# Kernel optimization log

Measured on AMD Instinct MI355X. Metric: run time of the kernel, lower is better.

## Reference

```python
import jax, jax.numpy as jnp
import numpy as np

HW = 16          # feature map side before crop
P = HW * HW      # 256 spatial positions
G = 128          # output genetic channels per branch
CROP = 14        # crop size


def feature_genetic(x, idx, oh, ow):
    # x: [B, C, 16, 16]; idx: [G, P] channel index per (group, position);
    # oh, ow: [G] crop offsets in {0,1}
    B = x.shape[0]
    feat = x.reshape(B, x.shape[1], P)                 # [B, C, 256]
    pos = jnp.arange(P)
    picked = feat[:, idx, pos]                         # [B, G, 256]
    grid = picked.reshape(B, G, HW, HW)                # [B, 128, 16, 16]
    ch = jnp.arange(G)
    hidx = oh[:, None] + jnp.arange(CROP)[None, :]     # [G, 14]
    widx = ow[:, None] + jnp.arange(CROP)[None, :]     # [G, 14]
    # fancy-index crop: [B, 128, 14, 14]
    return grid[:, ch[:, None, None], hidx[:, :, None], widx[:, None, :]]


def setup_inputs() -> dict:
    key = jax.random.key(0)
    k1, k3, k5, kw, ki, kh, kw2 = jax.random.split(key, 7)
    B, C = 128, 512
    x1 = jax.random.normal(k1, (B, C, HW, HW), dtype=jnp.float32)
    x3 = jax.random.normal(k3, (B, C, HW, HW), dtype=jnp.float32)
    x5 = jax.random.normal(k5, (B, C, HW, HW), dtype=jnp.float32)
    W = jax.random.normal(kw, (768, 384), dtype=jnp.float32) * 0.02  # 1x1 conv weight
    idx = jax.random.randint(ki, (3, G, P), 0, C, dtype=jnp.int32)
    offh = jax.random.randint(kh, (3, G), 0, 2, dtype=jnp.int32)
    offw = jax.random.randint(kw2, (3, G), 0, 2, dtype=jnp.int32)
    return {"x1": x1, "x3": x3, "x5": x5, "W": W, "idx": idx, "offh": offh, "offw": offw}


def reference(x1, x3, x5, W, idx, offh, offw):
    g1 = feature_genetic(x1, idx[0], offh[0], offw[0])   # [B, 128, 14, 14]
    g3 = feature_genetic(x3, idx[1], offh[1], offw[1])
    g5 = feature_genetic(x5, idx[2], offh[2], offw[2])
    feats = jnp.concatenate((g1, g3, g5), axis=1)        # [B, 384, 14, 14]
    # 1x1 conv (no bias): Conv2d(384, 768, kernel_size=1)
    out = jnp.einsum('bchw,oc->bohw', feats, W)          # [B, 768, 14, 14]
    return out
```

## Files before the change

kernel.cpp:

```cpp
#include <hip/hip_runtime.h>
#include <hip/hip_bf16.h>

#define PIX 256
#define CROP 14
#define HW2 196
#define BB 128
#define CC 512
#define NC 384
#define NO 768
#define CAP 128
#define ENT_T 25088

typedef __bf16 bf16x8 __attribute__((ext_vector_type(8)));
typedef __bf16 bf16x4 __attribute__((ext_vector_type(4)));
typedef float  f32x4  __attribute__((ext_vector_type(4)));
typedef unsigned int u32;

#define GLOAD_LDS16(src, dst) \
    __builtin_amdgcn_global_load_lds((const __attribute__((address_space(1))) void*)(src), \
                                     (__attribute__((address_space(3))) void*)(dst), 16, 0, 0)

__global__ void wconv_kernel(const float* __restrict__ W, __bf16* __restrict__ Wb) {
    int tid = blockIdx.x * 256 + threadIdx.x;
    Wb[tid] = (__bf16)W[tid];
}

__global__ void fill_kernel(const int* __restrict__ idx, const int* __restrict__ offh,
                            const int* __restrict__ offw, int* __restrict__ cnt,
                            u32* __restrict__ bucket) {
    int tid = blockIdx.x * 256 + threadIdx.x;
    int c3 = tid / HW2;
    int hw = tid - c3 * HW2;
    int i = hw / CROP, j = hw - i * CROP;
    int p = (offh[c3] + i) * 16 + offw[c3] + j;
    int ch = idx[c3 * PIX + p];
    int bkt = (c3 >> 7) * CC + ch;
    int pos = atomicAdd(&cnt[bkt], 1);
    if (pos < CAP)
        bucket[bkt * CAP + pos] =
            ((u32)(c3 & 127) << 25) | ((u32)hw << 17) | ((u32)p << 9) | (u32)ch;
}

__global__ __launch_bounds__(256) void scan_kernel(const int* __restrict__ cnt,
                                                   int* __restrict__ pref) {
    __shared__ int part[256];
    int tid = threadIdx.x;
    int loc[6];
    int s = 0;
#pragma unroll
    for (int i = 0; i < 6; ++i) {
        int v = cnt[tid * 6 + i]; if (v > CAP) v = CAP;
        loc[i] = s; s += v;
    }
    part[tid] = s;
    __syncthreads();
    if (tid < 64) {
        int l4[4]; int s4 = 0;
#pragma unroll
        for (int i = 0; i < 4; ++i) { l4[i] = s4; s4 += part[tid * 4 + i]; }
        int v = s4;
#pragma unroll
        for (int d = 1; d < 64; d <<= 1) { int u = __shfl_up(v, d); if (tid >= d) v += u; }
        int excl = v - s4;
#pragma unroll
        for (int i = 0; i < 4; ++i) part[tid * 4 + i] = excl + l4[i];
    }
    __syncthreads();
    int off = part[tid];
#pragma unroll
    for (int i = 0; i < 6; ++i) pref[tid * 6 + i] = off + loc[i];
}

__global__ __launch_bounds__(128) void compact_kernel(const int* __restrict__ cnt,
                                                      const int* __restrict__ pref,
                                                      const u32* __restrict__ bucket,
                                                      u32* __restrict__ ent) {
    int bkt = blockIdx.x;
    int E = cnt[bkt]; if (E > CAP) E = CAP;
    int tid = threadIdx.x;
    if (tid < E) ent[pref[bkt] + tid] = bucket[bkt * CAP + tid];
}

__global__ __launch_bounds__(256) void scatter_kernel(
        const float* __restrict__ x1, const float* __restrict__ x3,
        const float* __restrict__ x5, const u32* __restrict__ ent,
        __bf16* __restrict__ feats) {
    __shared__ __bf16 fl[HW2 * 128];
    int blk = blockIdx.x;
    int b = blk / 3;
    int t = blk - b * 3;
    const float* x = (t == 0) ? x1 : (t == 1) ? x3 : x5;
    const float* xb = x + (size_t)b * CC * PIX;
    const u32* el = ent + t * ENT_T;
    int tid = threadIdx.x;

#pragma unroll 4
    for (int g = tid; g < ENT_T; g += 256) {
        u32 wd = el[g];
        int ch = wd & 511;
        int p  = (wd >> 9) & 255;
        int hw = (wd >> 17) & 255;
        int c3 = wd >> 25;
        float f = xb[ch * PIX + p];
        fl[hw * 128 + c3] = (__bf16)f;
    }
    __syncthreads();

    const size_t obase = (size_t)b * HW2 * NC + (size_t)t * 128;
#pragma unroll 4
    for (int i2 = tid; i2 < HW2 * 32; i2 += 256) {
        int hw = i2 >> 5, cq = (i2 & 31) * 4;
        *(bf16x4*)(feats + obase + (size_t)hw * NC + cq) = *(const bf16x4*)&fl[hw * 128 + cq];
    }
}

__global__ __launch_bounds__(256) void gemm_kernel(const __bf16* __restrict__ feats,
                                                   const __bf16* __restrict__ Wb,
                                                   float* __restrict__ out) {
    __shared__ __bf16 ldsbuf[16384];
    __bf16* Abuf = ldsbuf;
    __bf16* Bbuf = ldsbuf + 8192;

    const int d = blockIdx.x;
    const int wg = (d & 7) * 147 + (d >> 3);
    const int o_base = (wg % 6) * 128;
    const int m_base = (wg / 6) * 128;

    const int tid = threadIdx.x;
    const int wave = tid >> 6, lane = tid & 63;
    const int wo = wave >> 1, wm = wave & 1;
    const int l15 = lane & 15, g = lane >> 4;
    const int xr = l15 & 7;

    f32x4 acc[4][4] = {};

    for (int kt = 0; kt < 6; ++kt) {
        const int k0g = kt * 64;
#pragma unroll
        for (int it = 0; it < 4; ++it) {
            int ck = tid + it * 256;
            int row = ck >> 3, cc = ck & 7;
            int koff = k0g + ((cc ^ (row & 7)) << 3);
            GLOAD_LDS16(Wb    + (size_t)(o_base + row) * NC + koff, Abuf + ck * 8);
            GLOAD_LDS16(feats + (size_t)(m_base + row) * NC + koff, Bbuf + ck * 8);
        }
        __syncthreads();
#pragma unroll
        for (int k0 = 0; k0 < 64; k0 += 32) {
            const int cb = (k0 >> 3) + g;
            bf16x8 a[4], b[4];
#pragma unroll
            for (int s = 0; s < 4; ++s) {
                int arow = wo * 64 + s * 16 + l15;
                a[s] = *(const bf16x8*)&Abuf[arow * 64 + ((cb ^ xr) << 3)];
                int brow = wm * 64 + s * 16 + l15;
                b[s] = *(const bf16x8*)&Bbuf[brow * 64 + ((cb ^ xr) << 3)];
            }
#pragma unroll
            for (int os = 0; os < 4; ++os)
#pragma unroll
                for (int ms = 0; ms < 4; ++ms)
                    acc[os][ms] = __builtin_amdgcn_mfma_f32_16x16x32_bf16(a[os], b[ms], acc[os][ms], 0, 0, 0);
        }
        __syncthreads();
    }

#pragma unroll
    for (int os = 0; os < 4; ++os)
#pragma unroll
        for (int ms = 0; ms < 4; ++ms) {
            int m = m_base + wm * 64 + ms * 16 + l15;
            int bb = m / HW2;
            int hw = m - bb * HW2;
            int o = o_base + wo * 64 + os * 16 + g * 4;
            float* dst = out + ((size_t)bb * NO + o) * HW2 + hw;
            f32x4 v = acc[os][ms];
            dst[0 * HW2] = v[0];
            dst[1 * HW2] = v[1];
            dst[2 * HW2] = v[2];
            dst[3 * HW2] = v[3];
        }
}

extern "C" void kernel_launch(void* const* d_in, const int* in_sizes, int n_in,
                              void* d_out, int out_size, void* d_ws, size_t ws_size,
                              hipStream_t stream) {
    const float* x1   = (const float*)d_in[0];
    const float* x3   = (const float*)d_in[1];
    const float* x5   = (const float*)d_in[2];
    const float* W    = (const float*)d_in[3];
    const int*   idx  = (const int*)d_in[4];
    const int*   offh = (const int*)d_in[5];
    const int*   offw = (const int*)d_in[6];
    float* out = (float*)d_out;

    char* ws = (char*)d_ws;
    __bf16* feats  = (__bf16*)(ws);
    __bf16* Wb     = (__bf16*)(ws + 19267584);
    int*    cnt    = (int*)   (ws + 19857408);
    int*    pref   = (int*)   (ws + 19863552);
    u32*    bucket = (u32*)   (ws + 19869696);
    u32*    ent    = (u32*)   (ws + 20656128);

    wconv_kernel<<<(NO * NC) / 256, 256, 0, stream>>>(W, Wb);
    hipMemsetAsync(cnt, 0, 1536 * sizeof(int), stream);
    fill_kernel<<<(NC * HW2) / 256, 256, 0, stream>>>(idx, offh, offw, cnt, bucket);
    scan_kernel<<<1, 256, 0, stream>>>(cnt, pref);
    compact_kernel<<<1536, 128, 0, stream>>>(cnt, pref, bucket, ent);
    scatter_kernel<<<384, 256, 0, stream>>>(x1, x3, x5, ent, feats);
    gemm_kernel<<<1176, 256, 0, stream>>>(feats, Wb, out);
}
```

Baseline: 107.7 us.

## Split gather-scatter into many small blocks writing bf16 directly to global

Each scatter block used to handle one whole (batch, branch) pair and stage results in a shared-memory tile before vectorized writes. It now launches 49 blocks per batch, and each thread gathers six entries in registers and writes single bf16 values straight to the feature matrix. The goal is more blocks and more loads in flight, so gather latency is hidden better. The cost is uncoalesced 2-byte global stores in place of 8-byte vector writes.

```diff
diff --git a/kernel.cpp b/kernel.cpp
--- a/kernel.cpp
+++ b/kernel.cpp
@@ -85,32 +85,32 @@
         const float* __restrict__ x1, const float* __restrict__ x3,
         const float* __restrict__ x5, const u32* __restrict__ ent,
         __bf16* __restrict__ feats) {
-    __shared__ __bf16 fl[HW2 * 128];
     int blk = blockIdx.x;
-    int b = blk / 3;
-    int t = blk - b * 3;
-    const float* x = (t == 0) ? x1 : (t == 1) ? x3 : x5;
-    const float* xb = x + (size_t)b * CC * PIX;
-    const u32* el = ent + t * ENT_T;
+    int b = blk / 49, c = blk - b * 49;
     int tid = threadIdx.x;
-
-#pragma unroll 4
-    for (int g = tid; g < ENT_T; g += 256) {
-        u32 wd = el[g];
-        int ch = wd & 511;
-        int p  = (wd >> 9) & 255;
-        int hw = (wd >> 17) & 255;
-        int c3 = wd >> 25;
-        float f = xb[ch * PIX + p];
-        fl[hw * 128 + c3] = (__bf16)f;
+    int e0 = c * 1536 + tid * 6;
+
+    u32 wd[6];
+#pragma unroll
+    for (int k = 0; k < 6; ++k) wd[k] = ent[e0 + k];
+
+    float f[6];
+    const size_t boff = (size_t)b * CC * PIX;
+#pragma unroll
+    for (int k = 0; k < 6; ++k) {
+        int e = e0 + k;
+        const float* x = (e >= 2 * ENT_T) ? x5 : (e >= ENT_T ? x3 : x1);
+        f[k] = x[boff + (size_t)((wd[k] & 511) * PIX + ((wd[k] >> 9) & 255))];
     }
     __syncthreads();
 
-    const size_t obase = (size_t)b * HW2 * NC + (size_t)t * 128;
-#pragma unroll 4
-    for (int i2 = tid; i2 < HW2 * 32; i2 += 256) {
-        int hw = i2 >> 5, cq = (i2 & 31) * 4;
-        *(bf16x4*)(feats + obase + (size_t)hw * NC + cq) = *(const bf16x4*)&fl[hw * 128 + cq];
+    const size_t fb = (size_t)b * HW2 * NC;
+#pragma unroll
+    for (int k = 0; k < 6; ++k) {
+        int e = e0 + k;
+        int t = (e >= 2 * ENT_T) ? 2 : (e >= ENT_T ? 1 : 0);
+        size_t col = (size_t)t * 128 + (wd[k] >> 25);
+        feats[fb + (size_t)((wd[k] >> 17) & 255) * NC + col] = (__bf16)f[k];
     }
 }
 
@@ -207,6 +207,6 @@
     fill_kernel<<<(NC * HW2) / 256, 256, 0, stream>>>(idx, offh, offw, cnt, bucket);
     scan_kernel<<<1, 256, 0, stream>>>(cnt, pref);
     compact_kernel<<<1536, 128, 0, stream>>>(cnt, pref, bucket, ent);
-    scatter_kernel<<<384, 256, 0, stream>>>(x1, x3, x5, ent, feats);
+    scatter_kernel<<<128 * 49, 256, 0, stream>>>(x1, x3, x5, ent, feats);
     gemm_kernel<<<1176, 256, 0, stream>>>(feats, Wb, out);
 }
```

After: 159.7 us. +48.3%, slower.

## Split gather-scatter into spatial quarters for more blocks and smaller LDS

Applied to the files above, without the earlier changes.

Buckets are now keyed by spatial quarter (49 positions each) as well as branch and channel, so each scatter block handles one batch, branch and quarter. The scatter launch grows from 384 to 1536 blocks with a quarter-size LDS tile, and writes out through 16-byte vectors with an XCD-aware block remap. This is meant to raise occupancy and parallelism in the memory-bound gather stage. The cost is a larger bucket, count and prefix setup: four times the counters, a heavier single-block scan and more compact blocks.

```diff
diff --git a/kernel.cpp b/kernel.cpp
--- a/kernel.cpp
+++ b/kernel.cpp
@@ -9,10 +9,9 @@
 #define NC 384
 #define NO 768
 #define CAP 128
-#define ENT_T 25088
+#define EQ 6272
 
 typedef __bf16 bf16x8 __attribute__((ext_vector_type(8)));
-typedef __bf16 bf16x4 __attribute__((ext_vector_type(4)));
 typedef float  f32x4  __attribute__((ext_vector_type(4)));
 typedef unsigned int u32;
 
@@ -34,7 +33,8 @@
     int i = hw / CROP, j = hw - i * CROP;
     int p = (offh[c3] + i) * 16 + offw[c3] + j;
     int ch = idx[c3 * PIX + p];
-    int bkt = (c3 >> 7) * CC + ch;
+    int q = hw / 49;
+    int bkt = (c3 >> 7) * 2048 + q * 512 + ch;
     int pos = atomicAdd(&cnt[bkt], 1);
     if (pos < CAP)
         bucket[bkt * CAP + pos] =
@@ -45,11 +45,11 @@
                                                    int* __restrict__ pref) {
     __shared__ int part[256];
     int tid = threadIdx.x;
-    int loc[6];
+    int loc[24];
     int s = 0;
 #pragma unroll
-    for (int i = 0; i < 6; ++i) {
-        int v = cnt[tid * 6 + i]; if (v > CAP) v = CAP;
+    for (int i = 0; i < 24; ++i) {
+        int v = cnt[tid * 24 + i]; if (v > CAP) v = CAP;
         loc[i] = s; s += v;
     }
     part[tid] = s;
@@ -68,7 +68,7 @@
     __syncthreads();
     int off = part[tid];
 #pragma unroll
-    for (int i = 0; i < 6; ++i) pref[tid * 6 + i] = off + loc[i];
+    for (int i = 0; i < 24; ++i) pref[tid * 24 + i] = off + loc[i];
 }
 
 __global__ __launch_bounds__(128) void compact_kernel(const int* __restrict__ cnt,
@@ -85,32 +85,31 @@
         const float* __restrict__ x1, const float* __restrict__ x3,
         const float* __restrict__ x5, const u32* __restrict__ ent,
         __bf16* __restrict__ feats) {
-    __shared__ __bf16 fl[HW2 * 128];
-    int blk = blockIdx.x;
-    int b = blk / 3;
-    int t = blk - b * 3;
+    __shared__ __bf16 fl[49 * 128];
+    int d = blockIdx.x;
+    int wg = (d & 7) * 192 + (d >> 3);
+    int b = wg / 12, tq = wg - b * 12;
+    int t = tq >> 2, q = tq & 3;
     const float* x = (t == 0) ? x1 : (t == 1) ? x3 : x5;
     const float* xb = x + (size_t)b * CC * PIX;
-    const u32* el = ent + t * ENT_T;
+    const u32* el = ent + tq * EQ;
     int tid = threadIdx.x;
 
-#pragma unroll 4
-    for (int g = tid; g < ENT_T; g += 256) {
+    for (int g = tid; g < EQ; g += 256) {
         u32 wd = el[g];
         int ch = wd & 511;
         int p  = (wd >> 9) & 255;
         int hw = (wd >> 17) & 255;
         int c3 = wd >> 25;
         float f = xb[ch * PIX + p];
-        fl[hw * 128 + c3] = (__bf16)f;
+        fl[(hw - q * 49) * 128 + c3] = (__bf16)f;
     }
     __syncthreads();
 
-    const size_t obase = (size_t)b * HW2 * NC + (size_t)t * 128;
-#pragma unroll 4
-    for (int i2 = tid; i2 < HW2 * 32; i2 += 256) {
-        int hw = i2 >> 5, cq = (i2 & 31) * 4;
-        *(bf16x4*)(feats + obase + (size_t)hw * NC + cq) = *(const bf16x4*)&fl[hw * 128 + cq];
+    const size_t obase = ((size_t)b * HW2 + q * 49) * NC + (size_t)t * 128;
+    for (int i2 = tid; i2 < 49 * 16; i2 += 256) {
+        int hwl = i2 >> 4, ck = (i2 & 15) * 8;
+        *(bf16x8*)(feats + obase + (size_t)hwl * NC + ck) = *(const bf16x8*)&fl[hwl * 128 + ck];
     }
 }
 
@@ -198,15 +197,15 @@
     __bf16* feats  = (__bf16*)(ws);
     __bf16* Wb     = (__bf16*)(ws + 19267584);
     int*    cnt    = (int*)   (ws + 19857408);
-    int*    pref   = (int*)   (ws + 19863552);
-    u32*    bucket = (u32*)   (ws + 19869696);
-    u32*    ent    = (u32*)   (ws + 20656128);
+    int*    pref   = (int*)   (ws + 19881984);
+    u32*    bucket = (u32*)   (ws + 19906560);
+    u32*    ent    = (u32*)   (ws + 23052288);
 
     wconv_kernel<<<(NO * NC) / 256, 256, 0, stream>>>(W, Wb);
-    hipMemsetAsync(cnt, 0, 1536 * sizeof(int), stream);
+    hipMemsetAsync(cnt, 0, 6144 * sizeof(int), stream);
     fill_kernel<<<(NC * HW2) / 256, 256, 0, stream>>>(idx, offh, offw, cnt, bucket);
     scan_kernel<<<1, 256, 0, stream>>>(cnt, pref);
-    compact_kernel<<<1536, 128, 0, stream>>>(cnt, pref, bucket, ent);
-    scatter_kernel<<<384, 256, 0, stream>>>(x1, x3, x5, ent, feats);
+    compact_kernel<<<6144, 128, 0, stream>>>(cnt, pref, bucket, ent);
+    scatter_kernel<<<1536, 256, 0, stream>>>(x1, x3, x5, ent, feats);
     gemm_kernel<<<1176, 256, 0, stream>>>(feats, Wb, out);
 }
```

After: 97.66 us. 9.3% less time.

## Stream channel slabs into LDS and scatter picked values directly to feats

Applied to the files above, without the earlier changes.

The scatter kernel now splits each (batch, branch) into eight 64-channel slabs over 3072 blocks. Each block loads its slab with coalesced float4 reads, converts it to bf16 in LDS, and walks only the sorted entries whose channel falls in that slab, writing each value straight into feats. This replaces random per-entry global gathers with a dense streaming read and adds parallelism. The cost is that all of x is read rather than only the picked elements, and the output writes become scattered 2-byte stores. The memset of the counters is also folded into the weight-conversion kernel, which removes one launch.

```diff
diff --git a/kernel.cpp b/kernel.cpp
--- a/kernel.cpp
+++ b/kernel.cpp
@@ -9,7 +9,6 @@
 #define NC 384
 #define NO 768
 #define CAP 128
-#define ENT_T 25088
 
 typedef __bf16 bf16x8 __attribute__((ext_vector_type(8)));
 typedef __bf16 bf16x4 __attribute__((ext_vector_type(4)));
@@ -20,9 +19,11 @@
     __builtin_amdgcn_global_load_lds((const __attribute__((address_space(1))) void*)(src), \
                                      (__attribute__((address_space(3))) void*)(dst), 16, 0, 0)
 
-__global__ void wconv_kernel(const float* __restrict__ W, __bf16* __restrict__ Wb) {
+__global__ void wconv_kernel(const float* __restrict__ W, __bf16* __restrict__ Wb,
+                             int* __restrict__ cnt) {
     int tid = blockIdx.x * 256 + threadIdx.x;
     Wb[tid] = (__bf16)W[tid];
+    if (tid < 1536) cnt[tid] = 0;
 }
 
 __global__ void fill_kernel(const int* __restrict__ idx, const int* __restrict__ offh,
@@ -34,7 +35,7 @@
     int i = hw / CROP, j = hw - i * CROP;
     int p = (offh[c3] + i) * 16 + offw[c3] + j;
     int ch = idx[c3 * PIX + p];
-    int bkt = (c3 >> 7) * CC + ch;
+    int bkt = (c3 >> 7) * 512 + ch;
     int pos = atomicAdd(&cnt[bkt], 1);
     if (pos < CAP)
         bucket[bkt * CAP + pos] =
@@ -84,33 +85,38 @@
 __global__ __launch_bounds__(256) void scatter_kernel(
         const float* __restrict__ x1, const float* __restrict__ x3,
         const float* __restrict__ x5, const u32* __restrict__ ent,
-        __bf16* __restrict__ feats) {
-    __shared__ __bf16 fl[HW2 * 128];
-    int blk = blockIdx.x;
-    int b = blk / 3;
-    int t = blk - b * 3;
+        const int* __restrict__ pref, __bf16* __restrict__ feats) {
+    __shared__ __bf16 fl[64 * 256];
+    int d = blockIdx.x;
+    int wg = (d & 7) * 384 + (d >> 3);
+    int b = wg / 24, tq = wg - b * 24;
+    int t = tq >> 3, oct = tq & 7;
     const float* x = (t == 0) ? x1 : (t == 1) ? x3 : x5;
-    const float* xb = x + (size_t)b * CC * PIX;
-    const u32* el = ent + t * ENT_T;
+    const float* base = x + ((size_t)b * CC + oct * 64) * PIX;
     int tid = threadIdx.x;
 
 #pragma unroll 4
-    for (int g = tid; g < ENT_T; g += 256) {
-        u32 wd = el[g];
+    for (int i = 0; i < 16; ++i) {
+        int fo = i * 1024 + tid * 4;
+        f32x4 v = *(const f32x4*)(base + fo);
+        bf16x4 q;
+        q[0] = (__bf16)v[0]; q[1] = (__bf16)v[1];
+        q[2] = (__bf16)v[2]; q[3] = (__bf16)v[3];
+        *(bf16x4*)&fl[fo] = q;
+    }
+    __syncthreads();
+
+    int pi = t * 512 + oct * 64;
+    int e0 = pref[pi];
+    int e1 = (pi + 64 >= 1536) ? 75264 : pref[pi + 64];
+    const size_t fb = (size_t)b * HW2 * NC + (size_t)t * 128;
+    for (int g = e0 + tid; g < e1; g += 256) {
+        u32 wd = ent[g];
         int ch = wd & 511;
         int p  = (wd >> 9) & 255;
         int hw = (wd >> 17) & 255;
         int c3 = wd >> 25;
-        float f = xb[ch * PIX + p];
-        fl[hw * 128 + c3] = (__bf16)f;
-    }
-    __syncthreads();
-
-    const size_t obase = (size_t)b * HW2 * NC + (size_t)t * 128;
-#pragma unroll 4
-    for (int i2 = tid; i2 < HW2 * 32; i2 += 256) {
-        int hw = i2 >> 5, cq = (i2 & 31) * 4;
-        *(bf16x4*)(feats + obase + (size_t)hw * NC + cq) = *(const bf16x4*)&fl[hw * 128 + cq];
+        feats[fb + (size_t)hw * NC + c3] = fl[(ch & 63) * 256 + p];
     }
 }
 
@@ -202,11 +208,10 @@
     u32*    bucket = (u32*)   (ws + 19869696);
     u32*    ent    = (u32*)   (ws + 20656128);
 
-    wconv_kernel<<<(NO * NC) / 256, 256, 0, stream>>>(W, Wb);
-    hipMemsetAsync(cnt, 0, 1536 * sizeof(int), stream);
+    wconv_kernel<<<(NO * NC) / 256, 256, 0, stream>>>(W, Wb, cnt);
     fill_kernel<<<(NC * HW2) / 256, 256, 0, stream>>>(idx, offh, offw, cnt, bucket);
     scan_kernel<<<1, 256, 0, stream>>>(cnt, pref);
     compact_kernel<<<1536, 128, 0, stream>>>(cnt, pref, bucket, ent);
-    scatter_kernel<<<384, 256, 0, stream>>>(x1, x3, x5, ent, feats);
+    scatter_kernel<<<3072, 256, 0, stream>>>(x1, x3, x5, ent, pref, feats);
     gemm_kernel<<<1176, 256, 0, stream>>>(feats, Wb, out);
 }
```

After: 131.7 us. 22.2% more time.
